# Optimization experiments

Measured on AMD Instinct MI355X. Metric: run time of the kernel, lower is better.

## Reference

```python
import jax, jax.numpy as jnp
import numpy as np

T, B, IN, H, OUT, L = 2048, 128, 64, 128, 32, 2


def setup_inputs() -> dict:
    key = jax.random.key(0)
    ks = jax.random.split(key, 8)
    s_in = 1.0 / np.sqrt(H)  # torch LSTM init scale: U(-1/sqrt(H), 1/sqrt(H))
    inp = {
        "x": jax.random.normal(ks[0], (T, B, IN), dtype=jnp.float32),
        "w_ih0": jax.random.uniform(ks[1], (4 * H, IN), minval=-s_in, maxval=s_in, dtype=jnp.float32),
        "w_hh0": jax.random.uniform(ks[2], (4 * H, H), minval=-s_in, maxval=s_in, dtype=jnp.float32),
        "w_ih1": jax.random.uniform(ks[3], (4 * H, H), minval=-s_in, maxval=s_in, dtype=jnp.float32),
        "w_hh1": jax.random.uniform(ks[4], (4 * H, H), minval=-s_in, maxval=s_in, dtype=jnp.float32),
        "fc_w": jax.random.uniform(ks[5], (OUT, H), minval=-s_in, maxval=s_in, dtype=jnp.float32),
        "fc_b": jax.random.uniform(ks[6], (OUT,), minval=-s_in, maxval=s_in, dtype=jnp.float32),
    }
    return inp


def _lstm_layer(x, w_ih, w_hh):
    # x: [T, B, D]; gate order i, f, g, o (PyTorch convention), no bias.
    x_proj = jnp.einsum("tbd,gd->tbg", x, w_ih)  # [T, B, 4H] precomputed input GEMM
    h0 = jnp.zeros((x.shape[1], H), dtype=x.dtype)
    c0 = jnp.zeros((x.shape[1], H), dtype=x.dtype)

    def step(carry, xp):
        h, c = carry
        gates = xp + h @ w_hh.T  # [B, 4H]
        i, f, g, o = jnp.split(gates, 4, axis=-1)
        i = jax.nn.sigmoid(i)
        f = jax.nn.sigmoid(f)
        g = jnp.tanh(g)
        o = jax.nn.sigmoid(o)
        c = f * c + i * g
        h = o * jnp.tanh(c)
        return (h, c), h

    (h_n, c_n), ys = jax.lax.scan(step, (h0, c0), x_proj)
    return ys, h_n, c_n


def reference(x, w_ih0, w_hh0, w_ih1, w_hh1, fc_w, fc_b):
    y0, h0n, c0n = _lstm_layer(x, w_ih0, w_hh0)
    y1, h1n, c1n = _lstm_layer(y0, w_ih1, w_hh1)
    out = jnp.einsum("tbh,oh->tbo", y1, fc_w) + fc_b  # [T, B, OUT]
    h_n = jnp.stack([h0n, h1n], axis=0)  # [L, B, H]
    c_n = jnp.stack([c0n, c1n], axis=0)
    return out, (h_n, c_n)
```

## Files before the change

### kernel.cpp

```cpp
#include <hip/hip_runtime.h>

#define T_ 2048
#define B_ 128
#define IN_ 64
#define H_ 128
#define OUT_ 32
#define CH_ 32
#define RING_ 2

typedef _Float16 half8 __attribute__((ext_vector_type(8)));
typedef _Float16 half4v __attribute__((ext_vector_type(4)));
typedef float float4v __attribute__((ext_vector_type(4)));

#define XSTR 144
#define HSTR 272
#define GRP_ELEMS ((size_t)RING_ * CH_ * 16 * 128)
#define RING_BYTES ((size_t)8 * GRP_ELEMS * 2)

#define NLOG2E  (-1.4426950408889634f)
#define C2LOG2E ( 2.8853900817779268f)

__device__ __forceinline__ float exp2_hw(float x) {
#if __has_builtin(__builtin_amdgcn_exp2f)
  return __builtin_amdgcn_exp2f(x);
#else
  return exp2f(x);
#endif
}
__device__ __forceinline__ float sigm_pre(float xs) {
  return __builtin_amdgcn_rcpf(1.0f + exp2_hw(xs));
}
__device__ __forceinline__ float tanh_pre(float xs) {
  return fmaf(-2.0f, __builtin_amdgcn_rcpf(1.0f + exp2_hw(xs)), 1.0f);
}
__device__ __forceinline__ float tanh_c(float x) { return tanh_pre(x * C2LOG2E); }

__device__ __forceinline__ float4v sigm4(float4v a) {
  float4v r;
#pragma unroll
  for (int i = 0; i < 4; ++i) r[i] = sigm_pre(a[i]);
  return r;
}
__device__ __forceinline__ float4v tanh4(float4v a) {
  float4v r;
#pragma unroll
  for (int i = 0; i < 4; ++i) r[i] = tanh_pre(a[i]);
  return r;
}

__device__ __forceinline__ half8 make_afrag(const float* __restrict__ W, int K, int row, int col, float sc) {
  const float* p = W + (size_t)row * K + col;
  float4 a = *(const float4*)p;
  float4 b = *(const float4*)(p + 4);
  half8 h;
  h[0]=(_Float16)(a.x*sc); h[1]=(_Float16)(a.y*sc); h[2]=(_Float16)(a.z*sc); h[3]=(_Float16)(a.w*sc);
  h[4]=(_Float16)(b.x*sc); h[5]=(_Float16)(b.y*sc); h[6]=(_Float16)(b.z*sc); h[7]=(_Float16)(b.w*sc);
  return h;
}

__device__ __forceinline__ void wait_ge(int* p, int want) {
  while (__hip_atomic_load(p, __ATOMIC_RELAXED, __HIP_MEMORY_SCOPE_AGENT) < want)
    __builtin_amdgcn_s_sleep(2);
}

__global__ void ring_init(int* f) { if (threadIdx.x < 16) f[threadIdx.x] = 0; }

__global__ __launch_bounds__(512) void lstm_wavefront(
    const float* __restrict__ x, const float* __restrict__ w_ih0,
    const float* __restrict__ w_hh0, const float* __restrict__ w_ih1,
    const float* __restrict__ w_hh1, const float* __restrict__ fc_w,
    const float* __restrict__ fc_b, float* __restrict__ out, char* __restrict__ ws)
{
  const int tid  = threadIdx.x, lane = tid & 63, w = tid >> 6;
  const int quad = lane >> 4, n = lane & 15;
  const int g = blockIdx.x & 7, layer = blockIdx.x >> 3;
  _Float16* ring = (_Float16*)ws + (size_t)g * GRP_ELEMS;
  int* flag     = (int*)(ws + RING_BYTES) + g;
  int* consumed = (int*)(ws + RING_BYTES) + 8 + g;

  __shared__ char sh_x[4 * 16 * XSTR];
  __shared__ char sh_h[8 * 16 * HSTR];

  const size_t hn_base = (size_t)T_ * B_ * OUT_;
  float4v c = {0.f, 0.f, 0.f, 0.f};
  float hf[4] = {0.f, 0.f, 0.f, 0.f};

  for (int i = tid; i < 8 * 16 * HSTR / 4; i += 512) ((unsigned*)sh_h)[i] = 0u;

  if (layer == 0) {
    half8 a_x[4][2], a_h[4][4];
#pragma unroll
    for (int gt = 0; gt < 4; ++gt) {
      const float sc = (gt == 2) ? C2LOG2E : NLOG2E;
      const int row = gt * H_ + w * 16 + n;
#pragma unroll
      for (int kt = 0; kt < 2; ++kt) a_x[gt][kt] = make_afrag(w_ih0, IN_, row, kt * 32 + quad * 8, sc);
#pragma unroll
      for (int kt = 0; kt < 4; ++kt) a_h[gt][kt] = make_afrag(w_hh0, H_, row, kt * 32 + quad * 8, sc);
    }
    const int xn = tid >> 5, xk = (tid & 31) * 2;
    {
#pragma unroll
      for (int k = 0; k < 2; ++k) {
        float2 xv = *(const float2*)(x + ((size_t)k * B_ + g * 16 + xn) * IN_ + xk);
        _Float16* d = (_Float16*)(sh_x + k * 16 * XSTR + xn * XSTR + xk * 2);
        d[0] = (_Float16)xv.x; d[1] = (_Float16)xv.y;
      }
    }
    __syncthreads();
    float4v accI[4];
    {
      half8 Bx[2];
#pragma unroll
      for (int kt = 0; kt < 2; ++kt)
        Bx[kt] = *(const half8*)(sh_x + n * XSTR + (kt * 32 + quad * 8) * 2);
#pragma unroll
      for (int gt = 0; gt < 4; ++gt) {
        float4v a0 = {0.f, 0.f, 0.f, 0.f};
        a0 = __builtin_amdgcn_mfma_f32_16x16x32_f16(a_x[gt][0], Bx[0], a0, 0, 0, 0);
        a0 = __builtin_amdgcn_mfma_f32_16x16x32_f16(a_x[gt][1], Bx[1], a0, 0, 0, 0);
        accI[gt] = a0;
      }
    }
    half4v hh_def = {0, 0, 0, 0};

    for (int t = 0; t < T_; ++t) {
      const int ck = t >> 5, s = t & (CH_ - 1);
      if (s == 0 && ck >= RING_) wait_ge(consumed, ck - 1);
      if (t > 0)
        *(half4v*)(ring + ((size_t)((t - 1) & 63) * 16 + n) * 128 + w * 16 + quad * 4) = hh_def;
      float2 xv = make_float2(0.f, 0.f);
      if (t + 2 < T_) xv = *(const float2*)(x + ((size_t)(t + 2) * B_ + g * 16 + xn) * IN_ + xk);

      half8 Bh[4];
#pragma unroll
      for (int kt = 0; kt < 4; ++kt)
        Bh[kt] = *(const half8*)(sh_h + ((t - 1) & 7) * 16 * HSTR + n * HSTR + (kt * 32 + quad * 8) * 2);

      float4v ga[4];
#pragma unroll
      for (int gt = 0; gt < 4; ++gt) {
        float4v acc = accI[gt];
#pragma unroll
        for (int kt = 0; kt < 4; ++kt)
          acc = __builtin_amdgcn_mfma_f32_16x16x32_f16(a_h[gt][kt], Bh[kt], acc, 0, 0, 0);
        ga[gt] = (gt == 2) ? tanh4(acc) : sigm4(acc);
      }
      if (t + 1 < T_) {
        half8 Bx[2];
#pragma unroll
        for (int kt = 0; kt < 2; ++kt)
          Bx[kt] = *(const half8*)(sh_x + ((t + 1) & 3) * 16 * XSTR + n * XSTR + (kt * 32 + quad * 8) * 2);
#pragma unroll
        for (int gt = 0; gt < 4; ++gt) {
          float4v a0 = {0.f, 0.f, 0.f, 0.f};
          a0 = __builtin_amdgcn_mfma_f32_16x16x32_f16(a_x[gt][0], Bx[0], a0, 0, 0, 0);
          a0 = __builtin_amdgcn_mfma_f32_16x16x32_f16(a_x[gt][1], Bx[1], a0, 0, 0, 0);
          accI[gt] = a0;
        }
      }
      half4v hh;
#pragma unroll
      for (int r = 0; r < 4; ++r) {
        c[r] = fmaf(ga[1][r], c[r], ga[0][r] * ga[2][r]);
        hf[r] = ga[3][r] * tanh_c(c[r]);
        hh[r] = (_Float16)hf[r];
      }
      *(half4v*)(sh_h + (t & 7) * 16 * HSTR + n * HSTR + (w * 16 + quad * 4) * 2) = hh;
      hh_def = hh;
      if (t + 2 < T_) {
        _Float16* d = (_Float16*)(sh_x + ((t + 2) & 3) * 16 * XSTR + xn * XSTR + xk * 2);
        d[0] = (_Float16)xv.x; d[1] = (_Float16)xv.y;
      }
      __syncthreads();
      if (tid == 0 && s == 0 && t > 0) {
        __builtin_amdgcn_fence(__ATOMIC_RELEASE, "agent");
        __hip_atomic_store(flag, ck, __ATOMIC_RELAXED, __HIP_MEMORY_SCOPE_AGENT);
      }
    }
    *(half4v*)(ring + ((size_t)((T_ - 1) & 63) * 16 + n) * 128 + w * 16 + quad * 4) = hh_def;
    __syncthreads();
    if (tid == 0) {
      __builtin_amdgcn_fence(__ATOMIC_RELEASE, "agent");
      __hip_atomic_store(flag, T_ / CH_, __ATOMIC_RELAXED, __HIP_MEMORY_SCOPE_AGENT);
    }
    {
      float* hn = out + hn_base;
      float* cn = out + hn_base + 2 * (size_t)B_ * H_;
      size_t idx = (size_t)(g * 16 + n) * H_ + w * 16 + quad * 4;
      *(float4*)(hn + idx) = make_float4(hf[0], hf[1], hf[2], hf[3]);
      *(float4*)(cn + idx) = make_float4(c[0], c[1], c[2], c[3]);
    }
  } else {
    half8 a_i[4][4], a_h[4][4], a_fc[4];
#pragma unroll
    for (int gt = 0; gt < 4; ++gt) {
      const float sc = (gt == 2) ? C2LOG2E : NLOG2E;
      const int row = gt * H_ + w * 16 + n;
#pragma unroll
      for (int kt = 0; kt < 4; ++kt) {
        a_i[gt][kt] = make_afrag(w_ih1, H_, row, kt * 32 + quad * 8, sc);
        a_h[gt][kt] = make_afrag(w_hh1, H_, row, kt * 32 + quad * 8, sc);
      }
    }
#pragma unroll
    for (int kt = 0; kt < 4; ++kt)
      a_fc[kt] = make_afrag(fc_w, H_, (w & 1) * 16 + n, kt * 32 + quad * 8, 1.0f);
    const float4 fb = *(const float4*)(fc_b + (w & 1) * 16 + quad * 4);
    __syncthreads();

    float4v accI[4];
#pragma unroll
    for (int gt = 0; gt < 4; ++gt) accI[gt] = (float4v){0.f, 0.f, 0.f, 0.f};

    for (int t = 0; t < T_; ++t) {
      const int ck = t >> 5, s = t & (CH_ - 1);
      if (s == 0) {
        wait_ge(flag, ck + 1);
        __builtin_amdgcn_fence(__ATOMIC_ACQUIRE, "agent");
        const _Float16* yp = ring + ((size_t)(t & 63) * 16 + n) * 128 + quad * 8;
        half8 By[4];
#pragma unroll
        for (int kt = 0; kt < 4; ++kt) By[kt] = *(const half8*)(yp + kt * 32);
#pragma unroll
        for (int gt = 0; gt < 4; ++gt) {
          float4v a0 = {0.f, 0.f, 0.f, 0.f};
#pragma unroll
          for (int kt = 0; kt < 4; ++kt)
            a0 = __builtin_amdgcn_mfma_f32_16x16x32_f16(a_i[gt][kt], By[kt], a0, 0, 0, 0);
          accI[gt] = a0;
        }
      }
      half8 Bh[4];
#pragma unroll
      for (int kt = 0; kt < 4; ++kt)
        Bh[kt] = *(const half8*)(sh_h + ((t - 1) & 7) * 16 * HSTR + n * HSTR + (kt * 32 + quad * 8) * 2);

      float4v ga[4];
#pragma unroll
      for (int gt = 0; gt < 4; ++gt) {
        float4v acc = accI[gt];
#pragma unroll
        for (int kt = 0; kt < 4; ++kt)
          acc = __builtin_amdgcn_mfma_f32_16x16x32_f16(a_h[gt][kt], Bh[kt], acc, 0, 0, 0);
        ga[gt] = (gt == 2) ? tanh4(acc) : sigm4(acc);
      }
      if (s != CH_ - 1) {
        const _Float16* yp = ring + ((size_t)((t + 1) & 63) * 16 + n) * 128 + quad * 8;
        half8 By[4];
#pragma unroll
        for (int kt = 0; kt < 4; ++kt) By[kt] = *(const half8*)(yp + kt * 32);
#pragma unroll
        for (int gt = 0; gt < 4; ++gt) {
          float4v a0 = {0.f, 0.f, 0.f, 0.f};
#pragma unroll
          for (int kt = 0; kt < 4; ++kt)
            a0 = __builtin_amdgcn_mfma_f32_16x16x32_f16(a_i[gt][kt], By[kt], a0, 0, 0, 0);
          accI[gt] = a0;
        }
      }
      half4v hh;
#pragma unroll
      for (int r = 0; r < 4; ++r) {
        c[r] = fmaf(ga[1][r], c[r], ga[0][r] * ga[2][r]);
        hf[r] = ga[3][r] * tanh_c(c[r]);
        hh[r] = (_Float16)hf[r];
      }
      *(half4v*)(sh_h + (t & 7) * 16 * HSTR + n * HSTR + (w * 16 + quad * 4) * 2) = hh;
      __syncthreads();
      if (s == CH_ - 1 && tid == 0) {
        __builtin_amdgcn_fence(__ATOMIC_RELEASE, "agent");
        __hip_atomic_store(consumed, ck + 1, __ATOMIC_RELAXED, __HIP_MEMORY_SCOPE_AGENT);
      }
      if ((t & 3) == 3) {
        const int sj = t - 3 + (w >> 1);
        half8 Bf[4];
#pragma unroll
        for (int kt = 0; kt < 4; ++kt)
          Bf[kt] = *(const half8*)(sh_h + (sj & 7) * 16 * HSTR + n * HSTR + (kt * 32 + quad * 8) * 2);
        float4v af = {0.f, 0.f, 0.f, 0.f};
#pragma unroll
        for (int kt = 0; kt < 4; ++kt)
          af = __builtin_amdgcn_mfma_f32_16x16x32_f16(a_fc[kt], Bf[kt], af, 0, 0, 0);
        float* op = out + ((size_t)sj * B_ + g * 16 + n) * OUT_ + (w & 1) * 16 + quad * 4;
        *(float4*)op = make_float4(af[0] + fb.x, af[1] + fb.y, af[2] + fb.z, af[3] + fb.w);
      }
    }
    {
      float* hn = out + hn_base + (size_t)B_ * H_;
      float* cn = out + hn_base + 3 * (size_t)B_ * H_;
      size_t idx = (size_t)(g * 16 + n) * H_ + w * 16 + quad * 4;
      *(float4*)(hn + idx) = make_float4(hf[0], hf[1], hf[2], hf[3]);
      *(float4*)(cn + idx) = make_float4(c[0], c[1], c[2], c[3]);
    }
  }
}

extern "C" void kernel_launch(void* const* d_in, const int* in_sizes, int n_in,
                              void* d_out, int out_size, void* d_ws, size_t ws_size,
                              hipStream_t stream) {
  const float* x     = (const float*)d_in[0];
  const float* w_ih0 = (const float*)d_in[1];
  const float* w_hh0 = (const float*)d_in[2];
  const float* w_ih1 = (const float*)d_in[3];
  const float* w_hh1 = (const float*)d_in[4];
  const float* fc_w  = (const float*)d_in[5];
  const float* fc_b  = (const float*)d_in[6];
  char* ws = (char*)d_ws;
  ring_init<<<1, 64, 0, stream>>>((int*)(ws + RING_BYTES));
  lstm_wavefront<<<16, 512, 0, stream>>>(x, w_ih0, w_hh0, w_ih1, w_hh1,
                                         fc_w, fc_b, (float*)d_out, ws);
}
```

Baseline: 3.358 ms.

## Use lightweight barriers, double-buffer h, and fold input GEMM into recurrent chain

Replaces __syncthreads with custom barriers that wait only on LDS counters, except once per chunk where a full vmcnt wait is needed before publishing the ring flag. Shrinks the h history buffer from 8 slots to 2 and moves the FC output projection into every step, run by two waves on the just-read h tile instead of batched every 4 steps. The input-projection MFMAs are now computed inside the per-step gate chain rather than precomputed for the next step, which lengthens the serial MFMA dependency but cuts barrier cost and register pressure. Ring loads for the next step are still prefetched into registers.

```diff
diff --git a/kernel.cpp b/kernel.cpp
--- a/kernel.cpp
+++ b/kernel.cpp
@@ -46,6 +46,21 @@
 #pragma unroll
   for (int i = 0; i < 4; ++i) r[i] = tanh_pre(a[i]);
   return r;
+}
+
+__device__ __forceinline__ void bar_light() {
+  __builtin_amdgcn_sched_barrier(0);
+  asm volatile("s_waitcnt lgkmcnt(0)" ::: "memory");
+  __builtin_amdgcn_s_barrier();
+  asm volatile("" ::: "memory");
+  __builtin_amdgcn_sched_barrier(0);
+}
+__device__ __forceinline__ void bar_full() {
+  __builtin_amdgcn_sched_barrier(0);
+  asm volatile("s_waitcnt vmcnt(0) lgkmcnt(0)" ::: "memory");
+  __builtin_amdgcn_s_barrier();
+  asm volatile("" ::: "memory");
+  __builtin_amdgcn_sched_barrier(0);
 }
 
 __device__ __forceinline__ half8 make_afrag(const float* __restrict__ W, int K, int row, int col, float sc) {
@@ -79,13 +94,13 @@
   int* consumed = (int*)(ws + RING_BYTES) + 8 + g;
 
   __shared__ char sh_x[4 * 16 * XSTR];
-  __shared__ char sh_h[8 * 16 * HSTR];
+  __shared__ char sh_h[2 * 16 * HSTR];
 
   const size_t hn_base = (size_t)T_ * B_ * OUT_;
   float4v c = {0.f, 0.f, 0.f, 0.f};
   float hf[4] = {0.f, 0.f, 0.f, 0.f};
 
-  for (int i = tid; i < 8 * 16 * HSTR / 4; i += 512) ((unsigned*)sh_h)[i] = 0u;
+  for (int i = tid; i < 2 * 16 * HSTR / 4; i += 512) ((unsigned*)sh_h)[i] = 0u;
 
   if (layer == 0) {
     half8 a_x[4][2], a_h[4][4];
@@ -99,29 +114,13 @@
       for (int kt = 0; kt < 4; ++kt) a_h[gt][kt] = make_afrag(w_hh0, H_, row, kt * 32 + quad * 8, sc);
     }
     const int xn = tid >> 5, xk = (tid & 31) * 2;
-    {
-#pragma unroll
-      for (int k = 0; k < 2; ++k) {
-        float2 xv = *(const float2*)(x + ((size_t)k * B_ + g * 16 + xn) * IN_ + xk);
-        _Float16* d = (_Float16*)(sh_x + k * 16 * XSTR + xn * XSTR + xk * 2);
-        d[0] = (_Float16)xv.x; d[1] = (_Float16)xv.y;
-      }
+#pragma unroll
+    for (int k = 0; k < 2; ++k) {
+      float2 xv = *(const float2*)(x + ((size_t)k * B_ + g * 16 + xn) * IN_ + xk);
+      _Float16* d = (_Float16*)(sh_x + k * 16 * XSTR + xn * XSTR + xk * 2);
+      d[0] = (_Float16)xv.x; d[1] = (_Float16)xv.y;
     }
     __syncthreads();
-    float4v accI[4];
-    {
-      half8 Bx[2];
-#pragma unroll
-      for (int kt = 0; kt < 2; ++kt)
-        Bx[kt] = *(const half8*)(sh_x + n * XSTR + (kt * 32 + quad * 8) * 2);
-#pragma unroll
-      for (int gt = 0; gt < 4; ++gt) {
-        float4v a0 = {0.f, 0.f, 0.f, 0.f};
-        a0 = __builtin_amdgcn_mfma_f32_16x16x32_f16(a_x[gt][0], Bx[0], a0, 0, 0, 0);
-        a0 = __builtin_amdgcn_mfma_f32_16x16x32_f16(a_x[gt][1], Bx[1], a0, 0, 0, 0);
-        accI[gt] = a0;
-      }
-    }
     half4v hh_def = {0, 0, 0, 0};
 
     for (int t = 0; t < T_; ++t) {
@@ -132,32 +131,24 @@
       float2 xv = make_float2(0.f, 0.f);
       if (t + 2 < T_) xv = *(const float2*)(x + ((size_t)(t + 2) * B_ + g * 16 + xn) * IN_ + xk);
 
-      half8 Bh[4];
+      half8 Bx[2], Bh[4];
+#pragma unroll
+      for (int kt = 0; kt < 2; ++kt)
+        Bx[kt] = *(const half8*)(sh_x + (t & 3) * 16 * XSTR + n * XSTR + (kt * 32 + quad * 8) * 2);
 #pragma unroll
       for (int kt = 0; kt < 4; ++kt)
-        Bh[kt] = *(const half8*)(sh_h + ((t - 1) & 7) * 16 * HSTR + n * HSTR + (kt * 32 + quad * 8) * 2);
+        Bh[kt] = *(const half8*)(sh_h + (t & 1) * 16 * HSTR + n * HSTR + (kt * 32 + quad * 8) * 2);
 
       float4v ga[4];
 #pragma unroll
       for (int gt = 0; gt < 4; ++gt) {
-        float4v acc = accI[gt];
+        float4v acc = {0.f, 0.f, 0.f, 0.f};
+        acc = __builtin_amdgcn_mfma_f32_16x16x32_f16(a_x[gt][0], Bx[0], acc, 0, 0, 0);
+        acc = __builtin_amdgcn_mfma_f32_16x16x32_f16(a_x[gt][1], Bx[1], acc, 0, 0, 0);
 #pragma unroll
         for (int kt = 0; kt < 4; ++kt)
           acc = __builtin_amdgcn_mfma_f32_16x16x32_f16(a_h[gt][kt], Bh[kt], acc, 0, 0, 0);
         ga[gt] = (gt == 2) ? tanh4(acc) : sigm4(acc);
-      }
-      if (t + 1 < T_) {
-        half8 Bx[2];
-#pragma unroll
-        for (int kt = 0; kt < 2; ++kt)
-          Bx[kt] = *(const half8*)(sh_x + ((t + 1) & 3) * 16 * XSTR + n * XSTR + (kt * 32 + quad * 8) * 2);
-#pragma unroll
-        for (int gt = 0; gt < 4; ++gt) {
-          float4v a0 = {0.f, 0.f, 0.f, 0.f};
-          a0 = __builtin_amdgcn_mfma_f32_16x16x32_f16(a_x[gt][0], Bx[0], a0, 0, 0, 0);
-          a0 = __builtin_amdgcn_mfma_f32_16x16x32_f16(a_x[gt][1], Bx[1], a0, 0, 0, 0);
-          accI[gt] = a0;
-        }
       }
       half4v hh;
 #pragma unroll
@@ -166,20 +157,20 @@
         hf[r] = ga[3][r] * tanh_c(c[r]);
         hh[r] = (_Float16)hf[r];
       }
-      *(half4v*)(sh_h + (t & 7) * 16 * HSTR + n * HSTR + (w * 16 + quad * 4) * 2) = hh;
+      *(half4v*)(sh_h + ((t & 1) ^ 1) * 16 * HSTR + n * HSTR + (w * 16 + quad * 4) * 2) = hh;
       hh_def = hh;
       if (t + 2 < T_) {
         _Float16* d = (_Float16*)(sh_x + ((t + 2) & 3) * 16 * XSTR + xn * XSTR + xk * 2);
         d[0] = (_Float16)xv.x; d[1] = (_Float16)xv.y;
       }
-      __syncthreads();
+      if (s == 0) bar_full(); else bar_light();
       if (tid == 0 && s == 0 && t > 0) {
         __builtin_amdgcn_fence(__ATOMIC_RELEASE, "agent");
         __hip_atomic_store(flag, ck, __ATOMIC_RELAXED, __HIP_MEMORY_SCOPE_AGENT);
       }
     }
     *(half4v*)(ring + ((size_t)((T_ - 1) & 63) * 16 + n) * 128 + w * 16 + quad * 4) = hh_def;
-    __syncthreads();
+    bar_full();
     if (tid == 0) {
       __builtin_amdgcn_fence(__ATOMIC_RELEASE, "agent");
       __hip_atomic_store(flag, T_ / CH_, __ATOMIC_RELAXED, __HIP_MEMORY_SCOPE_AGENT);
@@ -203,15 +194,14 @@
         a_h[gt][kt] = make_afrag(w_hh1, H_, row, kt * 32 + quad * 8, sc);
       }
     }
-#pragma unroll
-    for (int kt = 0; kt < 4; ++kt)
-      a_fc[kt] = make_afrag(fc_w, H_, (w & 1) * 16 + n, kt * 32 + quad * 8, 1.0f);
-    const float4 fb = *(const float4*)(fc_b + (w & 1) * 16 + quad * 4);
+    float4 fb = make_float4(0.f, 0.f, 0.f, 0.f);
+    if (w < 2) {
+#pragma unroll
+      for (int kt = 0; kt < 4; ++kt) a_fc[kt] = make_afrag(fc_w, H_, w * 16 + n, kt * 32 + quad * 8, 1.0f);
+      fb = *(const float4*)(fc_b + w * 16 + quad * 4);
+    }
     __syncthreads();
-
-    float4v accI[4];
-#pragma unroll
-    for (int gt = 0; gt < 4; ++gt) accI[gt] = (float4v){0.f, 0.f, 0.f, 0.f};
+    half8 By[4];
 
     for (int t = 0; t < T_; ++t) {
       const int ck = t >> 5, s = t & (CH_ - 1);
@@ -219,45 +209,39 @@
         wait_ge(flag, ck + 1);
         __builtin_amdgcn_fence(__ATOMIC_ACQUIRE, "agent");
         const _Float16* yp = ring + ((size_t)(t & 63) * 16 + n) * 128 + quad * 8;
-        half8 By[4];
 #pragma unroll
         for (int kt = 0; kt < 4; ++kt) By[kt] = *(const half8*)(yp + kt * 32);
-#pragma unroll
-        for (int gt = 0; gt < 4; ++gt) {
-          float4v a0 = {0.f, 0.f, 0.f, 0.f};
-#pragma unroll
-          for (int kt = 0; kt < 4; ++kt)
-            a0 = __builtin_amdgcn_mfma_f32_16x16x32_f16(a_i[gt][kt], By[kt], a0, 0, 0, 0);
-          accI[gt] = a0;
-        }
       }
       half8 Bh[4];
 #pragma unroll
       for (int kt = 0; kt < 4; ++kt)
-        Bh[kt] = *(const half8*)(sh_h + ((t - 1) & 7) * 16 * HSTR + n * HSTR + (kt * 32 + quad * 8) * 2);
-
+        Bh[kt] = *(const half8*)(sh_h + (t & 1) * 16 * HSTR + n * HSTR + (kt * 32 + quad * 8) * 2);
+      if (w < 2 && t > 0) {
+        float4v af = {0.f, 0.f, 0.f, 0.f};
+#pragma unroll
+        for (int kt = 0; kt < 4; ++kt)
+          af = __builtin_amdgcn_mfma_f32_16x16x32_f16(a_fc[kt], Bh[kt], af, 0, 0, 0);
+        float* op = out + ((size_t)(t - 1) * B_ + g * 16 + n) * OUT_ + w * 16 + quad * 4;
+        *(float4*)op = make_float4(af[0] + fb.x, af[1] + fb.y, af[2] + fb.z, af[3] + fb.w);
+      }
       float4v ga[4];
 #pragma unroll
       for (int gt = 0; gt < 4; ++gt) {
-        float4v acc = accI[gt];
+        float4v acc = {0.f, 0.f, 0.f, 0.f};
+#pragma unroll
+        for (int kt = 0; kt < 4; ++kt)
+          acc = __builtin_amdgcn_mfma_f32_16x16x32_f16(a_i[gt][kt], By[kt], acc, 0, 0, 0);
 #pragma unroll
         for (int kt = 0; kt < 4; ++kt)
           acc = __builtin_amdgcn_mfma_f32_16x16x32_f16(a_h[gt][kt], Bh[kt], acc, 0, 0, 0);
         ga[gt] = (gt == 2) ? tanh4(acc) : sigm4(acc);
       }
-      if (s != CH_ - 1) {
+      half8 Byn[4];
+      const bool pf = (s != CH_ - 1) && (t + 1 < T_);
+      if (pf) {
         const _Float16* yp = ring + ((size_t)((t + 1) & 63) * 16 + n) * 128 + quad * 8;
-        half8 By[4];
-#pragma unroll
-        for (int kt = 0; kt < 4; ++kt) By[kt] = *(const half8*)(yp + kt * 32);
-#pragma unroll
-        for (int gt = 0; gt < 4; ++gt) {
-          float4v a0 = {0.f, 0.f, 0.f, 0.f};
-#pragma unroll
-          for (int kt = 0; kt < 4; ++kt)
-            a0 = __builtin_amdgcn_mfma_f32_16x16x32_f16(a_i[gt][kt], By[kt], a0, 0, 0, 0);
-          accI[gt] = a0;
-        }
+#pragma unroll
+        for (int kt = 0; kt < 4; ++kt) Byn[kt] = *(const half8*)(yp + kt * 32);
       }
       half4v hh;
 #pragma unroll
@@ -266,25 +250,26 @@
         hf[r] = ga[3][r] * tanh_c(c[r]);
         hh[r] = (_Float16)hf[r];
       }
-      *(half4v*)(sh_h + (t & 7) * 16 * HSTR + n * HSTR + (w * 16 + quad * 4) * 2) = hh;
-      __syncthreads();
+      *(half4v*)(sh_h + ((t & 1) ^ 1) * 16 * HSTR + n * HSTR + (w * 16 + quad * 4) * 2) = hh;
+      bar_light();
       if (s == CH_ - 1 && tid == 0) {
         __builtin_amdgcn_fence(__ATOMIC_RELEASE, "agent");
         __hip_atomic_store(consumed, ck + 1, __ATOMIC_RELAXED, __HIP_MEMORY_SCOPE_AGENT);
       }
-      if ((t & 3) == 3) {
-        const int sj = t - 3 + (w >> 1);
-        half8 Bf[4];
-#pragma unroll
-        for (int kt = 0; kt < 4; ++kt)
-          Bf[kt] = *(const half8*)(sh_h + (sj & 7) * 16 * HSTR + n * HSTR + (kt * 32 + quad * 8) * 2);
-        float4v af = {0.f, 0.f, 0.f, 0.f};
-#pragma unroll
-        for (int kt = 0; kt < 4; ++kt)
-          af = __builtin_amdgcn_mfma_f32_16x16x32_f16(a_fc[kt], Bf[kt], af, 0, 0, 0);
-        float* op = out + ((size_t)sj * B_ + g * 16 + n) * OUT_ + (w & 1) * 16 + quad * 4;
-        *(float4*)op = make_float4(af[0] + fb.x, af[1] + fb.y, af[2] + fb.z, af[3] + fb.w);
-      }
+      if (pf) {
+#pragma unroll
+        for (int kt = 0; kt < 4; ++kt) By[kt] = Byn[kt];
+      }
+    }
+    if (w < 2) {
+      float4v af = {0.f, 0.f, 0.f, 0.f};
+#pragma unroll
+      for (int kt = 0; kt < 4; ++kt) {
+        half8 Bh = *(const half8*)(sh_h + (T_ & 1) * 16 * HSTR + n * HSTR + (kt * 32 + quad * 8) * 2);
+        af = __builtin_amdgcn_mfma_f32_16x16x32_f16(a_fc[kt], Bh, af, 0, 0, 0);
+      }
+      float* op = out + ((size_t)(T_ - 1) * B_ + g * 16 + n) * OUT_ + w * 16 + quad * 4;
+      *(float4*)op = make_float4(af[0] + fb.x, af[1] + fb.y, af[2] + fb.z, af[3] + fb.w);
     }
     {
       float* hn = out + hn_base + (size_t)B_ * H_;
```

New measurement: 2.938 ms. 1.14x faster.
